# Optimization experiments

Hardware: AMD Instinct MI355X
Metric: run time of the kernel (lower is better)

The kernel has to match this reference:

```python
import jax, jax.numpy as jnp
import numpy as np

SEQ = 4096
R_DIM = 1024
Z_DIM = 1024
AT_DIM = 1024
G_DIM = 1024


def _xavier(key, shape):
    fan_in, fan_out = shape[1], shape[0]
    limit = float(np.sqrt(6.0 / (fan_in + fan_out)))
    return jax.random.uniform(key, shape, jnp.float32, -limit, limit)


def setup_inputs() -> dict:
    key = jax.random.key(0)
    ks = jax.random.split(key, 12)
    return {
        "R": jax.random.normal(ks[0], (SEQ, R_DIM), jnp.float32),
        "W_alpha": _xavier(ks[1], (R_DIM, 2 * R_DIM)),
        "b_alpha": jnp.zeros((R_DIM,), jnp.float32),
        "W_delta": _xavier(ks[2], (R_DIM, 2 * R_DIM)),
        "b_delta": jnp.zeros((R_DIM,), jnp.float32),
        "W_q": _xavier(ks[3], (AT_DIM, Z_DIM)),
        "b_q": jnp.zeros((AT_DIM,), jnp.float32),
        "W_k": _xavier(ks[4], (AT_DIM, Z_DIM)),
        "b_k": jnp.zeros((AT_DIM,), jnp.float32),
        "W_v": _xavier(ks[5], (AT_DIM, Z_DIM)),
        "b_v": jnp.zeros((AT_DIM,), jnp.float32),
        "W_z": _xavier(ks[6], (Z_DIM, R_DIM)),
        "b_z": jnp.zeros((Z_DIM,), jnp.float32),
        "W_f": _xavier(ks[7], (AT_DIM, G_DIM)),
        "b_f": jnp.zeros((AT_DIM,), jnp.float32),
        "W_EMA": _xavier(ks[8], (G_DIM, R_DIM)),
        "b_EMA": jnp.zeros((G_DIM,), jnp.float32),
        "W_z_at": _xavier(ks[9], (G_DIM, AT_DIM)),
        "b_z_at": jnp.zeros((G_DIM,), jnp.float32),
        "W_i": _xavier(ks[10], (1, R_DIM)),
        "b_i": jnp.zeros((1,), jnp.float32),
        "W_final": _xavier(ks[11], (1, G_DIM)),
    }


def reference(R, W_alpha, b_alpha, W_delta, b_delta, W_q, b_q, W_k, b_k,
              W_v, b_v, W_z, b_z, W_f, b_f, W_EMA, b_EMA, W_z_at, b_z_at,
              W_i, b_i, W_final):
    r_dim = R.shape[-1]
    at_dim = W_q.shape[0]
    # prepend zero row; r_t / r_{t-1} pairs
    R2 = jnp.concatenate([jnp.zeros((1, r_dim), R.dtype), R], axis=0)
    r_t, r_prev = R2[1:], R2[:-1]
    concat_r = jnp.concatenate([r_prev, r_t], axis=1)  # [m, 2r]
    alpha = jnp.tanh(concat_r @ W_alpha.T + b_alpha)
    delta = jnp.tanh(concat_r @ W_delta.T + b_delta)
    R_EMA = alpha * r_t + (1.0 - alpha) * delta * r_prev
    Z = jax.nn.silu(R_EMA @ W_z.T + b_z)
    Q = Z @ W_q.T + b_q
    K = Z @ W_k.T + b_k
    V = Z @ W_v.T + b_v
    scores = (Q @ K.T) / jnp.sqrt(jnp.float32(at_dim))  # [m, m]
    weights = jax.nn.softmax(scores, axis=-1)
    Z_at = weights @ V
    R_EMA_p = R_EMA @ W_EMA.T + b_EMA
    f = jax.nn.sigmoid(R_EMA_p @ W_f.T + b_f)
    Z_at_p = f * Z_at
    Z_EMA_f = Z_at_p @ W_z_at.T + b_z_at
    Z_tp = jnp.tanh(R_EMA_p + Z_EMA_f)
    i = jnp.tanh(R_EMA @ W_i.T + b_i)  # [m, 1]
    Z_final = i * Z_tp + (1.0 - i) * R_EMA_p
    p_hat = jax.nn.sigmoid(Z_final @ W_final.T)  # [m, 1]
    return p_hat
```

## Files before the change

### kernel.cpp

```cpp
#include <hip/hip_runtime.h>
#include <cstdint>
#include <cmath>

#define MB (1024ull * 1024ull)

typedef unsigned short u16;
typedef __attribute__((ext_vector_type(8))) short short8;
typedef __attribute__((ext_vector_type(4))) float f32x4;

enum { M_TANH = 0, M_ZRE = 1, M_QKVF = 2, M_SCALE = 3, M_PVRAW = 4, M_F32 = 5 };

__device__ __forceinline__ u16 f2b(float f) {
  union { float f; uint32_t u; } v; v.f = f;
  uint32_t r = v.u + 0x7FFFu + ((v.u >> 16) & 1u);
  return (u16)(r >> 16);
}
__device__ __forceinline__ float b2f(u16 u) {
  union { uint32_t u; float f; } v; v.u = ((uint32_t)u) << 16;
  return v.f;
}

typedef __attribute__((address_space(3))) uint32_t lds_u32;
typedef const __attribute__((address_space(1))) uint32_t glb_u32;

__device__ __forceinline__ void gload16(const void* g, void* l) {
  __builtin_amdgcn_global_load_lds((glb_u32*)g, (lds_u32*)l, 16, 0, 0);
}

template <int MODE, int BMT, int BNT>
__global__ __launch_bounds__(256) void gemm(const u16* __restrict__ A,
                                            const u16* __restrict__ B,
                                            const float* __restrict__ bias,
                                            const u16* __restrict__ A2,
                                            const u16* __restrict__ B2,
                                            const float* __restrict__ bias2,
                                            u16* __restrict__ Cb,
                                            u16* __restrict__ Cb2,
                                            u16* __restrict__ Cb3,
                                            float* __restrict__ Cf,
                                            int K, int lda, int ldb, float scale) {
  constexpr int WN = (BMT == 64 && BNT == 128) ? 4 : 2;
  constexpr int WM = 4 / WN;
  constexpr int WR = BMT / WM;
  constexpr int WC = BNT / WN;
  constexpr int NI = WR / 16;
  constexpr int NJ = WC / 16;
  __shared__ u16 As[2][BMT * 32];
  __shared__ u16 Bs[2][BNT * 32];
  const int tid = threadIdx.x;
  const int wid = tid >> 6, lane = tid & 63;

  const int gx = gridDim.x, nwg = gx * gridDim.y;
  int id = blockIdx.y * gx + blockIdx.x;
  if ((nwg & 7) == 0) id = (id & 7) * (nwg >> 3) + (id >> 3);
  const int bm = (id / gx) * BMT, bn = (id % gx) * BNT;
  const int wm = wid / WN, wn = wid % WN;
  const int rowbase = wm * WR, colbase = wn * WC;

  const bool isf = (MODE == M_QKVF) && (bn >= 3072);
  const u16* Ab = isf ? A2 : A;
  const u16* Bb = isf ? B2 : B;
  const int bnl = isf ? bn - 3072 : bn;
  const int kofs = (MODE == M_PVRAW) ? (int)blockIdx.z * K : 0;

  const int srow = tid >> 2;
  const int schunk = (tid & 3) ^ ((srow >> 1) & 3);
  const u16* gA = Ab + (size_t)(bm + srow) * lda + kofs + schunk * 8;
  const u16* gB = Bb + (size_t)(bnl + srow) * ldb + kofs + schunk * 8;

  f32x4 acc[NI][NJ];
#pragma unroll
  for (int i = 0; i < NI; ++i)
#pragma unroll
    for (int j = 0; j < NJ; ++j) acc[i][j] = (f32x4){0.f, 0.f, 0.f, 0.f};

  const int ar = lane & 15;
  const int pch = (((lane >> 4) ^ ((ar >> 1) & 3))) * 8;

  const int NT = K >> 5;

  auto stage = [&](int buf, int t) {
    const u16* a = gA + (size_t)t * 32;
    const u16* b = gB + (size_t)t * 32;
    gload16(a, &As[buf][wid * 512]);
    if (BMT == 128) gload16(a + (size_t)64 * lda, &As[buf][wid * 512 + 2048]);
    gload16(b, &Bs[buf][wid * 512]);
    if (BNT == 128) gload16(b + (size_t)64 * ldb, &Bs[buf][wid * 512 + 2048]);
  };

  stage(0, 0);
  __syncthreads();
  int cur = 0;
  for (int t = 0; t < NT; ++t) {
    if (t + 1 < NT) stage(cur ^ 1, t + 1);
    short8 af[NI], bf[NJ];
#pragma unroll
    for (int i = 0; i < NI; ++i)
      af[i] = *reinterpret_cast<const short8*>(&As[cur][(rowbase + i * 16 + ar) * 32 + pch]);
#pragma unroll
    for (int j = 0; j < NJ; ++j)
      bf[j] = *reinterpret_cast<const short8*>(&Bs[cur][(colbase + j * 16 + ar) * 32 + pch]);
#pragma unroll
    for (int i = 0; i < NI; ++i)
#pragma unroll
      for (int j = 0; j < NJ; ++j)
        acc[i][j] = __builtin_amdgcn_mfma_f32_16x16x32_bf16(af[i], bf[j], acc[i][j], 0, 0, 0);
    __syncthreads();
    cur ^= 1;
  }

  float* Cfz = Cf;
  if (MODE == M_PVRAW && blockIdx.z != 0) Cfz = (float*)Cb3;

#pragma unroll
  for (int i = 0; i < NI; ++i) {
    const int rb = bm + rowbase + i * 16 + (lane >> 4) * 4;
#pragma unroll
    for (int j = 0; j < NJ; ++j) {
      const int n = bn + colbase + j * 16 + (lane & 15);
#pragma unroll
      for (int r = 0; r < 4; ++r) {
        const int m = rb + r;
        float v = acc[i][j][r];
        if (MODE == M_TANH) {
          v = tanhf(v + bias[n]);
          Cb[(size_t)m * 2048 + n] = f2b(v);
        } else if (MODE == M_ZRE) {
          v += bias[n];
          if (n < 1024) { const float s = v / (1.f + expf(-v)); Cb[(size_t)m * 1024 + n] = f2b(s); }
          else Cb2[(size_t)m * 1024 + (n - 1024)] = f2b(v);
        } else if (MODE == M_QKVF) {
          if (isf) {
            const int nl = n - 3072;
            const float s = 1.f / (1.f + expf(-(v + bias2[nl])));
            Cb3[(size_t)m * 1024 + nl] = f2b(s);
          } else {
            v += bias[n];
            if (n < 2048) Cb[(size_t)m * 2048 + n] = f2b(v);
            else Cb2[(size_t)m * 1024 + (n - 2048)] = f2b(v);
          }
        } else if (MODE == M_SCALE) {
          Cb[(size_t)m * 4096 + n] = f2b(v * scale);
        } else if (MODE == M_PVRAW) {
          Cfz[(size_t)m * 1024 + n] = v;
        } else if (MODE == M_F32) {
          Cf[(size_t)m * 1024 + n] = v + bias[n];
        }
      }
    }
  }
}

__global__ __launch_bounds__(256) void pv_reduce(const float* __restrict__ p0,
                                                 const float* __restrict__ p1,
                                                 const u16* __restrict__ fvb,
                                                 u16* __restrict__ Zatp) {
  const int idx = blockIdx.x * 256 + threadIdx.x;
  const float4 a = reinterpret_cast<const float4*>(p0)[idx];
  const float4 b = reinterpret_cast<const float4*>(p1)[idx];
  const ushort4 f4 = reinterpret_cast<const ushort4*>(fvb)[idx];
  ushort4 o;
  o.x = f2b((a.x + b.x) * b2f(f4.x));
  o.y = f2b((a.y + b.y) * b2f(f4.y));
  o.z = f2b((a.z + b.z) * b2f(f4.z));
  o.w = f2b((a.w + b.w) * b2f(f4.w));
  reinterpret_cast<ushort4*>(Zatp)[idx] = o;
}

__global__ __launch_bounds__(256) void convert_all(
    const float* __restrict__ s0, const float* __restrict__ s1, const float* __restrict__ s2,
    const float* __restrict__ s3, const float* __restrict__ s4, const float* __restrict__ s5,
    const float* __restrict__ s6, const float* __restrict__ s7, const float* __restrict__ s8,
    u16* __restrict__ Wad, u16* __restrict__ Wze, u16* __restrict__ Wqkv,
    u16* __restrict__ Wfb, u16* __restrict__ Wzab) {
  const int idx = blockIdx.x * 256 + threadIdx.x;
  const float* src; u16* dst; int off;
  if      (idx < 524288)  { src = s0; dst = Wad;           off = idx; }
  else if (idx < 1048576) { src = s1; dst = Wad + 2097152; off = idx - 524288; }
  else if (idx < 1310720) { src = s2; dst = Wze;           off = idx - 1048576; }
  else if (idx < 1572864) { src = s3; dst = Wze + 1048576; off = idx - 1310720; }
  else if (idx < 1835008) { src = s4; dst = Wqkv;          off = idx - 1572864; }
  else if (idx < 2097152) { src = s5; dst = Wqkv + 1048576; off = idx - 1835008; }
  else if (idx < 2359296) { src = s6; dst = Wqkv + 2097152; off = idx - 2097152; }
  else if (idx < 2621440) { src = s7; dst = Wfb;           off = idx - 2359296; }
  else                    { src = s8; dst = Wzab;          off = idx - 2621440; }
  const float4 v = reinterpret_cast<const float4*>(src)[off];
  ushort4 o; o.x = f2b(v.x); o.y = f2b(v.y); o.z = f2b(v.z); o.w = f2b(v.w);
  reinterpret_cast<ushort4*>(dst)[off] = o;
}

__global__ void copy_bias(const float* __restrict__ ba, const float* __restrict__ bd,
                          const float* __restrict__ bz, const float* __restrict__ be,
                          const float* __restrict__ bq, const float* __restrict__ bk,
                          const float* __restrict__ bv,
                          float* __restrict__ bad, float* __restrict__ bze,
                          float* __restrict__ bqkv) {
  const int t = threadIdx.x;
  const float4* src; float4* dst;
  switch (blockIdx.x) {
    case 0: src = (const float4*)ba; dst = (float4*)bad; break;
    case 1: src = (const float4*)bd; dst = (float4*)(bad + 1024); break;
    case 2: src = (const float4*)bz; dst = (float4*)bze; break;
    case 3: src = (const float4*)be; dst = (float4*)(bze + 1024); break;
    case 4: src = (const float4*)bq; dst = (float4*)bqkv; break;
    case 5: src = (const float4*)bk; dst = (float4*)(bqkv + 1024); break;
    default: src = (const float4*)bv; dst = (float4*)(bqkv + 2048); break;
  }
  dst[t] = src[t];
}

__global__ __launch_bounds__(256) void concat_kern(const float* __restrict__ R,
                                                   u16* __restrict__ Rc) {
  const int idx = blockIdx.x * 256 + threadIdx.x;
  const int m = idx >> 9;
  const int c = (idx & 511) * 4;
  float4 v;
  if (c < 1024) {
    if (m > 0) v = *reinterpret_cast<const float4*>(&R[(size_t)(m - 1) * 1024 + c]);
    else v = make_float4(0.f, 0.f, 0.f, 0.f);
  } else {
    v = *reinterpret_cast<const float4*>(&R[(size_t)m * 1024 + (c - 1024)]);
  }
  ushort4 o; o.x = f2b(v.x); o.y = f2b(v.y); o.z = f2b(v.z); o.w = f2b(v.w);
  reinterpret_cast<ushort4*>(Rc)[idx] = o;
}

__global__ __launch_bounds__(256) void ema_combine(const float* __restrict__ R,
                                                   const u16* __restrict__ adb,
                                                   u16* __restrict__ REMA) {
  const int idx = blockIdx.x * 256 + threadIdx.x;
  const int m = idx >> 8, c4 = idx & 255;
  const float4 rt = reinterpret_cast<const float4*>(R)[idx];
  float4 rp = make_float4(0.f, 0.f, 0.f, 0.f);
  if (m > 0) rp = reinterpret_cast<const float4*>(R)[idx - 256];
  const ushort4 a4 = reinterpret_cast<const ushort4*>(adb)[m * 512 + c4];
  const ushort4 d4 = reinterpret_cast<const ushort4*>(adb)[m * 512 + 256 + c4];
  ushort4 o;
  { const float av = b2f(a4.x); o.x = f2b(av * rt.x + (1.f - av) * b2f(d4.x) * rp.x); }
  { const float av = b2f(a4.y); o.y = f2b(av * rt.y + (1.f - av) * b2f(d4.y) * rp.y); }
  { const float av = b2f(a4.z); o.z = f2b(av * rt.z + (1.f - av) * b2f(d4.z) * rp.z); }
  { const float av = b2f(a4.w); o.w = f2b(av * rt.w + (1.f - av) * b2f(d4.w) * rp.w); }
  reinterpret_cast<ushort4*>(REMA)[idx] = o;
}

__device__ __forceinline__ float waveMax(float v) {
#pragma unroll
  for (int o = 32; o; o >>= 1) v = fmaxf(v, __shfl_down(v, o));
  return v;
}
__device__ __forceinline__ float waveSum(float v) {
#pragma unroll
  for (int o = 32; o; o >>= 1) v += __shfl_down(v, o);
  return v;
}

__global__ __launch_bounds__(256) void softmax_rows(u16* __restrict__ S) {
  u16* p = S + (size_t)blockIdx.x * 4096;
  const int tid = threadIdx.x;
  float v[16];
#pragma unroll
  for (int j = 0; j < 4; ++j) {
    const ushort4 t = *reinterpret_cast<const ushort4*>(&p[tid * 4 + 1024 * j]);
    v[4 * j + 0] = b2f(t.x); v[4 * j + 1] = b2f(t.y);
    v[4 * j + 2] = b2f(t.z); v[4 * j + 3] = b2f(t.w);
  }
  float mx = -INFINITY;
#pragma unroll
  for (int j = 0; j < 16; ++j) mx = fmaxf(mx, v[j]);
  __shared__ float red[4];
  const float wm = waveMax(mx);
  if ((tid & 63) == 0) red[tid >> 6] = wm;
  __syncthreads();
  mx = fmaxf(fmaxf(red[0], red[1]), fmaxf(red[2], red[3]));
  __syncthreads();
  float sum = 0.f;
#pragma unroll
  for (int j = 0; j < 16; ++j) { v[j] = expf(v[j] - mx); sum += v[j]; }
  const float ws_ = waveSum(sum);
  if ((tid & 63) == 0) red[tid >> 6] = ws_;
  __syncthreads();
  const float inv = 1.f / (red[0] + red[1] + red[2] + red[3]);
#pragma unroll
  for (int j = 0; j < 4; ++j) {
    ushort4 t;
    t.x = f2b(v[4 * j + 0] * inv); t.y = f2b(v[4 * j + 1] * inv);
    t.z = f2b(v[4 * j + 2] * inv); t.w = f2b(v[4 * j + 3] * inv);
    *reinterpret_cast<ushort4*>(&p[tid * 4 + 1024 * j]) = t;
  }
}

__global__ __launch_bounds__(256) void transpose_b16(const u16* __restrict__ V,
                                                     u16* __restrict__ Vt) {
  __shared__ u16 t[64][72];
  const int bn = blockIdx.x * 64;
  const int bk = blockIdx.y * 64;
  const int tx = threadIdx.x & 15, ty = threadIdx.x >> 4;
#pragma unroll
  for (int i = 0; i < 64; i += 16) {
    const ushort4 v = *reinterpret_cast<const ushort4*>(&V[(size_t)(bk + ty + i) * 1024 + bn + tx * 4]);
    t[ty + i][tx * 4 + 0] = v.x; t[ty + i][tx * 4 + 1] = v.y;
    t[ty + i][tx * 4 + 2] = v.z; t[ty + i][tx * 4 + 3] = v.w;
  }
  __syncthreads();
#pragma unroll
  for (int i = 0; i < 64; i += 16) {
    ushort4 w;
    w.x = t[tx * 4 + 0][ty + i]; w.y = t[tx * 4 + 1][ty + i];
    w.z = t[tx * 4 + 2][ty + i]; w.w = t[tx * 4 + 3][ty + i];
    *reinterpret_cast<ushort4*>(&Vt[(size_t)(bn + ty + i) * 4096 + bk + tx * 4]) = w;
  }
}

__global__ void final_kern(const u16* __restrict__ REMAb, const u16* __restrict__ REMApb,
                           const float* __restrict__ ZEMAf,
                           const float* __restrict__ Wi, const float* __restrict__ bi,
                           const float* __restrict__ Wfin, float* __restrict__ out) {
  const int m = blockIdx.x, l = threadIdx.x;
  float si = 0.f;
#pragma unroll
  for (int j = 0; j < 16; ++j) {
    const int n = l + 64 * j;
    si += b2f(REMAb[(size_t)m * 1024 + n]) * Wi[n];
  }
#pragma unroll
  for (int o = 32; o; o >>= 1) si += __shfl_xor(si, o);
  const float im = tanhf(si + bi[0]);
  float s = 0.f;
#pragma unroll
  for (int j = 0; j < 16; ++j) {
    const int n = l + 64 * j;
    const float rp = b2f(REMApb[(size_t)m * 1024 + n]);
    const float zf = im * tanhf(rp + ZEMAf[(size_t)m * 1024 + n]) + (1.f - im) * rp;
    s += zf * Wfin[n];
  }
#pragma unroll
  for (int o = 32; o; o >>= 1) s += __shfl_down(s, o);
  if (l == 0) out[m] = 1.f / (1.f + expf(-s));
}

extern "C" void kernel_launch(void* const* d_in, const int* in_sizes, int n_in,
                              void* d_out, int out_size, void* d_ws, size_t ws_size,
                              hipStream_t stream) {
  const float* R       = (const float*)d_in[0];
  const float* W_alpha = (const float*)d_in[1];  const float* b_alpha = (const float*)d_in[2];
  const float* W_delta = (const float*)d_in[3];  const float* b_delta = (const float*)d_in[4];
  const float* W_q     = (const float*)d_in[5];  const float* b_q     = (const float*)d_in[6];
  const float* W_k     = (const float*)d_in[7];  const float* b_k     = (const float*)d_in[8];
  const float* W_v     = (const float*)d_in[9];  const float* b_v     = (const float*)d_in[10];
  const float* W_z     = (const float*)d_in[11]; const float* b_z     = (const float*)d_in[12];
  const float* W_f     = (const float*)d_in[13]; const float* b_f     = (const float*)d_in[14];
  const float* W_EMA   = (const float*)d_in[15]; const float* b_EMA   = (const float*)d_in[16];
  const float* W_z_at  = (const float*)d_in[17]; const float* b_z_at  = (const float*)d_in[18];
  const float* W_i     = (const float*)d_in[19]; const float* b_i     = (const float*)d_in[20];
  const float* W_final = (const float*)d_in[21];
  float* out = (float*)d_out;
  uint8_t* w8 = (uint8_t*)d_ws;

  u16*   Rc     = (u16*)(w8 + 0 * MB);
  u16*   Zb     = (u16*)(w8 + 0 * MB);
  u16*   Zatpb  = (u16*)(w8 + 0 * MB);
  u16*   REMApb = (u16*)(w8 + 8 * MB);
  u16*   Wad    = (u16*)(w8 + 16 * MB);
  u16*   fvb    = (u16*)(w8 + 16 * MB);
  u16*   adb    = (u16*)(w8 + 24 * MB);
  float* pvp0   = (float*)(w8 + 24 * MB);
  float* ZEMAf  = (float*)(w8 + 24 * MB);
  u16*   Wqkv   = (u16*)(w8 + 40 * MB);
  u16*   Vtb    = (u16*)(w8 + 40 * MB);
  u16*   Wze    = (u16*)(w8 + 46 * MB);
  u16*   Wfb    = (u16*)(w8 + 50 * MB);
  u16*   Wzab   = (u16*)(w8 + 52 * MB);
  u16*   REMAb  = (u16*)(w8 + 54 * MB);
  u16*   QKb    = (u16*)(w8 + 62 * MB);
  float* pvp1   = (float*)(w8 + 62 * MB);
  u16*   Vb     = (u16*)(w8 + 78 * MB);
  u16*   Sb     = (u16*)(w8 + 78 * MB);
  float* bad    = (float*)(w8 + 110 * MB + 64 * 1024);
  float* bze    = bad + 2048;
  float* bqkv   = bze + 2048;

  const dim3 blk(256);
  convert_all<<<11264, blk, 0, stream>>>(W_alpha, W_delta, W_z, W_EMA, W_q, W_k, W_v, W_f, W_z_at,
                                         Wad, Wze, Wqkv, Wfb, Wzab);
  concat_kern<<<8192, blk, 0, stream>>>(R, Rc);
  copy_bias<<<7, blk, 0, stream>>>(b_alpha, b_delta, b_z, b_EMA, b_q, b_k, b_v, bad, bze, bqkv);

  gemm<M_TANH, 64, 128><<<dim3(16, 64), blk, 0, stream>>>(
      Rc, Wad, bad, nullptr, nullptr, nullptr, adb, nullptr, nullptr, nullptr, 2048, 2048, 2048, 1.f);
  ema_combine<<<4096, blk, 0, stream>>>(R, adb, REMAb);
  gemm<M_ZRE, 64, 128><<<dim3(16, 64), blk, 0, stream>>>(
      REMAb, Wze, bze, nullptr, nullptr, nullptr, Zb, REMApb, nullptr, nullptr, 1024, 1024, 1024, 1.f);
  gemm<M_QKVF, 64, 128><<<dim3(32, 64), blk, 0, stream>>>(
      Zb, Wqkv, bqkv, REMApb, Wfb, b_f, QKb, Vb, fvb, nullptr, 1024, 1024, 1024, 1.f);
  transpose_b16<<<dim3(16, 64), blk, 0, stream>>>(Vb, Vtb);
  gemm<M_SCALE, 128, 128><<<dim3(32, 32), blk, 0, stream>>>(
      QKb, QKb + 1024, nullptr, nullptr, nullptr, nullptr, Sb, nullptr, nullptr, nullptr, 1024, 2048, 2048, 0.03125f);
  softmax_rows<<<4096, blk, 0, stream>>>(Sb);
  gemm<M_PVRAW, 128, 64><<<dim3(16, 32, 2), blk, 0, stream>>>(
      Sb, Vtb, nullptr, nullptr, nullptr, nullptr, nullptr, nullptr, (u16*)pvp1, pvp0, 2048, 4096, 4096, 1.f);
  pv_reduce<<<4096, blk, 0, stream>>>(pvp0, pvp1, fvb, Zatpb);
  gemm<M_F32, 64, 128><<<dim3(8, 64), blk, 0, stream>>>(
      Zatpb, Wzab, b_z_at, nullptr, nullptr, nullptr, nullptr, nullptr, nullptr, ZEMAf, 1024, 1024, 1024, 1.f);
  final_kern<<<4096, 64, 0, stream>>>(REMAb, REMApb, ZEMAf, W_i, b_i, W_final, out);
}
```

Measured before the change: 340.7 us.

## Triple-buffer GEMM LDS pipeline with vmcnt waits and retile to 128-row blocks

```diff
diff --git a/kernel.cpp b/kernel.cpp
--- a/kernel.cpp
+++ b/kernel.cpp
@@ -27,7 +27,7 @@
   __builtin_amdgcn_global_load_lds((glb_u32*)g, (lds_u32*)l, 16, 0, 0);
 }
 
-template <int MODE, int BMT, int BNT>
+template <int MODE, int BNT>
 __global__ __launch_bounds__(256) void gemm(const u16* __restrict__ A,
                                             const u16* __restrict__ B,
                                             const float* __restrict__ bias,
@@ -39,23 +39,19 @@
                                             u16* __restrict__ Cb3,
                                             float* __restrict__ Cf,
                                             int K, int lda, int ldb, float scale) {
-  constexpr int WN = (BMT == 64 && BNT == 128) ? 4 : 2;
-  constexpr int WM = 4 / WN;
-  constexpr int WR = BMT / WM;
-  constexpr int WC = BNT / WN;
-  constexpr int NI = WR / 16;
-  constexpr int NJ = WC / 16;
-  __shared__ u16 As[2][BMT * 32];
-  __shared__ u16 Bs[2][BNT * 32];
+  constexpr int NI = 4;
+  constexpr int NJ = (BNT == 128) ? 4 : 2;
+  __shared__ u16 As[3][128 * 32];
+  __shared__ u16 Bs[3][BNT * 32];
   const int tid = threadIdx.x;
   const int wid = tid >> 6, lane = tid & 63;
 
   const int gx = gridDim.x, nwg = gx * gridDim.y;
   int id = blockIdx.y * gx + blockIdx.x;
   if ((nwg & 7) == 0) id = (id & 7) * (nwg >> 3) + (id >> 3);
-  const int bm = (id / gx) * BMT, bn = (id % gx) * BNT;
-  const int wm = wid / WN, wn = wid % WN;
-  const int rowbase = wm * WR, colbase = wn * WC;
+  const int bm = (id / gx) * 128, bn = (id % gx) * BNT;
+  const int wm = wid >> 1, wn = wid & 1;
+  const int rowbase = wm * 64, colbase = wn * (BNT / 2);
 
   const bool isf = (MODE == M_QKVF) && (bn >= 3072);
   const u16* Ab = isf ? A2 : A;
@@ -83,30 +79,39 @@
     const u16* a = gA + (size_t)t * 32;
     const u16* b = gB + (size_t)t * 32;
     gload16(a, &As[buf][wid * 512]);
-    if (BMT == 128) gload16(a + (size_t)64 * lda, &As[buf][wid * 512 + 2048]);
+    gload16(a + (size_t)64 * lda, &As[buf][wid * 512 + 2048]);
     gload16(b, &Bs[buf][wid * 512]);
     if (BNT == 128) gload16(b + (size_t)64 * ldb, &Bs[buf][wid * 512 + 2048]);
   };
 
   stage(0, 0);
-  __syncthreads();
-  int cur = 0;
+  stage(1, 1);
+  int cb = 0;
   for (int t = 0; t < NT; ++t) {
-    if (t + 1 < NT) stage(cur ^ 1, t + 1);
+    if (t + 1 < NT) {
+      if (BNT == 128) asm volatile("s_waitcnt vmcnt(4)" ::: "memory");
+      else            asm volatile("s_waitcnt vmcnt(3)" ::: "memory");
+    } else {
+      asm volatile("s_waitcnt vmcnt(0)" ::: "memory");
+    }
+    __builtin_amdgcn_s_barrier();
+    __builtin_amdgcn_sched_barrier(0);
+    if (t + 2 < NT) stage(cb == 0 ? 2 : cb - 1, t + 2);
     short8 af[NI], bf[NJ];
 #pragma unroll
     for (int i = 0; i < NI; ++i)
-      af[i] = *reinterpret_cast<const short8*>(&As[cur][(rowbase + i * 16 + ar) * 32 + pch]);
+      af[i] = *reinterpret_cast<const short8*>(&As[cb][(rowbase + i * 16 + ar) * 32 + pch]);
 #pragma unroll
     for (int j = 0; j < NJ; ++j)
-      bf[j] = *reinterpret_cast<const short8*>(&Bs[cur][(colbase + j * 16 + ar) * 32 + pch]);
+      bf[j] = *reinterpret_cast<const short8*>(&Bs[cb][(colbase + j * 16 + ar) * 32 + pch]);
+    __builtin_amdgcn_s_setprio(1);
 #pragma unroll
     for (int i = 0; i < NI; ++i)
 #pragma unroll
       for (int j = 0; j < NJ; ++j)
         acc[i][j] = __builtin_amdgcn_mfma_f32_16x16x32_bf16(af[i], bf[j], acc[i][j], 0, 0, 0);
-    __syncthreads();
-    cur ^= 1;
+    __builtin_amdgcn_s_setprio(0);
+    cb = (cb == 2) ? 0 : cb + 1;
   }
 
   float* Cfz = Cf;
@@ -385,21 +390,21 @@
   concat_kern<<<8192, blk, 0, stream>>>(R, Rc);
   copy_bias<<<7, blk, 0, stream>>>(b_alpha, b_delta, b_z, b_EMA, b_q, b_k, b_v, bad, bze, bqkv);
 
-  gemm<M_TANH, 64, 128><<<dim3(16, 64), blk, 0, stream>>>(
+  gemm<M_TANH, 128><<<dim3(16, 32), blk, 0, stream>>>(
       Rc, Wad, bad, nullptr, nullptr, nullptr, adb, nullptr, nullptr, nullptr, 2048, 2048, 2048, 1.f);
   ema_combine<<<4096, blk, 0, stream>>>(R, adb, REMAb);
-  gemm<M_ZRE, 64, 128><<<dim3(16, 64), blk, 0, stream>>>(
+  gemm<M_ZRE, 128><<<dim3(16, 32), blk, 0, stream>>>(
       REMAb, Wze, bze, nullptr, nullptr, nullptr, Zb, REMApb, nullptr, nullptr, 1024, 1024, 1024, 1.f);
-  gemm<M_QKVF, 64, 128><<<dim3(32, 64), blk, 0, stream>>>(
+  gemm<M_QKVF, 128><<<dim3(32, 32), blk, 0, stream>>>(
       Zb, Wqkv, bqkv, REMApb, Wfb, b_f, QKb, Vb, fvb, nullptr, 1024, 1024, 1024, 1.f);
   transpose_b16<<<dim3(16, 64), blk, 0, stream>>>(Vb, Vtb);
-  gemm<M_SCALE, 128, 128><<<dim3(32, 32), blk, 0, stream>>>(
+  gemm<M_SCALE, 128><<<dim3(32, 32), blk, 0, stream>>>(
       QKb, QKb + 1024, nullptr, nullptr, nullptr, nullptr, Sb, nullptr, nullptr, nullptr, 1024, 2048, 2048, 0.03125f);
   softmax_rows<<<4096, blk, 0, stream>>>(Sb);
-  gemm<M_PVRAW, 128, 64><<<dim3(16, 32, 2), blk, 0, stream>>>(
+  gemm<M_PVRAW, 128><<<dim3(8, 32, 2), blk, 0, stream>>>(
       Sb, Vtb, nullptr, nullptr, nullptr, nullptr, nullptr, nullptr, (u16*)pvp1, pvp0, 2048, 4096, 4096, 1.f);
   pv_reduce<<<4096, blk, 0, stream>>>(pvp0, pvp1, fvb, Zatpb);
-  gemm<M_F32, 64, 128><<<dim3(8, 64), blk, 0, stream>>>(
+  gemm<M_F32, 64><<<dim3(16, 32), blk, 0, stream>>>(
       Zatpb, Wzab, b_z_at, nullptr, nullptr, nullptr, nullptr, nullptr, nullptr, ZEMAf, 1024, 1024, 1024, 1.f);
   final_kern<<<4096, 64, 0, stream>>>(REMAb, REMApb, ZEMAf, W_i, b_i, W_final, out);
 }
```

Result: slower. 362.8 us (+6.5%).
